# Kernel optimization log

Measured on AMD Instinct MI355X. Metric: run time of the kernel, lower is better.

The kernel has to match this reference:

```python
import jax, jax.numpy as jnp
import numpy as np

# Fixed-step Dormand-Prince RK45 (dopri5) over t in [0, 1].
# torchdiffeq's dopri5 is adaptive; an adaptive while-loop is not
# reverse-differentiable in JAX, so we use the same dopri5 tableau with a
# fixed step count, which reproduces the per-step math exactly.
N_STEPS = 64

# dopri5 Butcher tableau (a-matrix rows; b = 5th-order weights = row a7)
A21 = 1/5
A31, A32 = 3/40, 9/40
A41, A42, A43 = 44/45, -56/15, 32/9
A51, A52, A53, A54 = 19372/6561, -25360/2187, 64448/6561, -212/729
A61, A62, A63, A64, A65 = 9017/3168, -355/33, 46732/5247, 49/176, -5103/18656
B1, B3, B4, B5, B6 = 35/384, 500/1113, 125/192, -2187/6784, 11/84


def setup_inputs() -> dict:
    key = jax.random.key(0)
    ks = jax.random.split(key, 7)
    data_dim, hidden_dim, batch = 512, 1024, 4096
    s1 = 1.0 / np.sqrt(data_dim)
    s2 = 1.0 / np.sqrt(hidden_dim)
    return {
        "x":  jax.random.normal(ks[0], (batch, data_dim), jnp.float32),
        "W1": jax.random.normal(ks[1], (hidden_dim, data_dim), jnp.float32) * s1,
        "b1": jax.random.normal(ks[2], (hidden_dim,), jnp.float32) * s1,
        "W2": jax.random.normal(ks[3], (hidden_dim, hidden_dim), jnp.float32) * s2,
        "b2": jax.random.normal(ks[4], (hidden_dim,), jnp.float32) * s2,
        "W3": jax.random.normal(ks[5], (data_dim, hidden_dim), jnp.float32) * s2,
        "b3": jax.random.normal(ks[6], (data_dim,), jnp.float32) * s2,
    }


def reference(x, W1, b1, W2, b2, W3, b3):
    def f(y):  # ODEFunc MLP: fc1 -> relu -> fc2 -> relu -> fc3 (autonomous)
        h = jax.nn.relu(y @ W1.T + b1)
        h = jax.nn.relu(h @ W2.T + b2)
        return h @ W3.T + b3

    h = jnp.float32(1.0 / N_STEPS)

    def step(y, _):
        k1 = f(y)
        k2 = f(y + h * (A21 * k1))
        k3 = f(y + h * (A31 * k1 + A32 * k2))
        k4 = f(y + h * (A41 * k1 + A42 * k2 + A43 * k3))
        k5 = f(y + h * (A51 * k1 + A52 * k2 + A53 * k3 + A54 * k4))
        k6 = f(y + h * (A61 * k1 + A62 * k2 + A63 * k3 + A64 * k4 + A65 * k5))
        y_next = y + h * (B1 * k1 + B3 * k3 + B4 * k4 + B5 * k5 + B6 * k6)
        return y_next, None

    y_final, _ = jax.lax.scan(step, x, None, length=N_STEPS)
    return y_final
```

## Files before the change

### kernel.cpp

```cpp
#include <hip/hip_runtime.h>
#include <hip/hip_bf16.h>
#include <stdint.h>
#include <stddef.h>

using bf16_t = __hip_bfloat16;
typedef __attribute__((ext_vector_type(8))) short short8;
typedef __attribute__((ext_vector_type(4))) float f32x4;

__device__ __forceinline__ void gload_lds16(void* lds, const void* g) {
  __builtin_amdgcn_global_load_lds(
      (const __attribute__((address_space(1))) unsigned int*)g,
      (__attribute__((address_space(3))) unsigned int*)lds,
      16, 0, 0);
}

template<int MFRAG, bool RELU, bool COMBINE, bool STORE_K, bool STORE_YF>
__global__ __launch_bounds__(256, 2)
void gemm_bt(const bf16_t* __restrict__ A, const bf16_t* __restrict__ B,
             const float* __restrict__ bias,
             bf16_t* __restrict__ obf,
             float* __restrict__ kout,
             float* __restrict__ yf_out,
             const float* __restrict__ y_in,
             const float* __restrict__ kp0, const float* __restrict__ kp1,
             const float* __restrict__ kp2, const float* __restrict__ kp3,
             float c0, float c1, float c2, float c3, float ccur,
             int M, int N, int K, int lgx)
{
  constexpr int BM = 32 * MFRAG;
  constexpr int BN = 64;
  constexpr int NFRAG = 2;
  constexpr int AR = BM / 32;
  constexpr int BR = 2;
  constexpr int LPT = AR + BR;

  __shared__ __align__(16) bf16_t As[3][BM * 64];
  __shared__ __align__(16) bf16_t Bs[3][BN * 64];

  const int t    = threadIdx.x;
  const int lane = t & 63;
  const int wid  = t >> 6;
  const int wm   = wid >> 1;
  const int wn   = wid & 1;

  const int nwg = gridDim.x;
  const int bid = blockIdx.x;
  const int swz = (bid & 7) * (nwg >> 3) + (bid >> 3);
  const int gxm = (1 << lgx) - 1;
  const int bx  = swz & gxm;
  const int by  = swz >> lgx;

  const int bn0 = bx * BN;
  const int bm0 = by * BM;

  const bf16_t* Ag = A + (size_t)bm0 * K;
  const bf16_t* Bg = B + (size_t)bn0 * K;

  f32x4 acc[MFRAG][NFRAG] = {};

  auto stage = [&](int b, int kt) {
    const int k0 = kt * 64;
#pragma unroll
    for (int r = 0; r < AR; ++r) {
      int ch  = t + r * 256;
      int row = ch >> 3, s = ch & 7;
      int sl  = s ^ (row & 7);
      gload_lds16(&As[b][ch * 8], Ag + (size_t)row * K + k0 + sl * 8);
    }
#pragma unroll
    for (int r = 0; r < BR; ++r) {
      int ch  = t + r * 256;
      int row = ch >> 3, s = ch & 7;
      int sl  = s ^ (row & 7);
      gload_lds16(&Bs[b][ch * 8], Bg + (size_t)row * K + k0 + sl * 8);
    }
  };

  const int nt = K >> 6;
  stage(0, 0);
  stage(1, 1);

  const int ro = lane & 15;
  const int ks = lane >> 4;

  int c = 0;
  for (int tt = 0; tt < nt; ++tt) {
    if (tt == nt - 1) {
      asm volatile("s_waitcnt vmcnt(0)" ::: "memory");
    } else if constexpr (LPT == 6) {
      asm volatile("s_waitcnt vmcnt(6)" ::: "memory");
    } else {
      asm volatile("s_waitcnt vmcnt(4)" ::: "memory");
    }
    __builtin_amdgcn_s_barrier();
    asm volatile("" ::: "memory");

#pragma unroll
    for (int kk = 0; kk < 2; ++kk) {
      short8 af[MFRAG], bfr[NFRAG];
      const int slot = kk * 4 + ks;
#pragma unroll
      for (int mi = 0; mi < MFRAG; ++mi) {
        int row = wm * (MFRAG * 16) + mi * 16 + ro;
        int ch  = row * 8 + (slot ^ (row & 7));
        af[mi]  = *(const short8*)&As[c][ch * 8];
      }
#pragma unroll
      for (int ni = 0; ni < NFRAG; ++ni) {
        int row = wn * 32 + ni * 16 + ro;
        int ch  = row * 8 + (slot ^ (row & 7));
        bfr[ni] = *(const short8*)&Bs[c][ch * 8];
      }
#pragma unroll
      for (int mi = 0; mi < MFRAG; ++mi)
#pragma unroll
        for (int ni = 0; ni < NFRAG; ++ni)
          acc[mi][ni] = __builtin_amdgcn_mfma_f32_16x16x32_bf16(
              af[mi], bfr[ni], acc[mi][ni], 0, 0, 0);
    }

    asm volatile("" ::: "memory");
    __builtin_amdgcn_s_barrier();
    asm volatile("" ::: "memory");

    if (tt + 2 < nt) {
      int nb = c + 2; if (nb >= 3) nb -= 3;
      stage(nb, tt + 2);
    }
    if (++c == 3) c = 0;
  }

  const int rb = bm0 + wm * (MFRAG * 16);
  const int cb = bn0 + wn * 32;
#pragma unroll
  for (int mi = 0; mi < MFRAG; ++mi) {
#pragma unroll
    for (int ni = 0; ni < NFRAG; ++ni) {
      const int col = cb + ni * 16 + (lane & 15);
      const float bv = bias[col];
#pragma unroll
      for (int r = 0; r < 4; ++r) {
        const int row = rb + mi * 16 + (lane >> 4) * 4 + r;
        const size_t idx = (size_t)row * N + col;
        float v = acc[mi][ni][r] + bv;
        if (RELU) v = fmaxf(v, 0.f);
        if (COMBINE) {
          if (STORE_K) kout[idx] = v;
          float z = y_in[idx] + ccur * v;
          if (kp0) z += c0 * kp0[idx];
          if (kp1) z += c1 * kp1[idx];
          if (kp2) z += c2 * kp2[idx];
          if (kp3) z += c3 * kp3[idx];
          if (STORE_YF) yf_out[idx] = z;
          obf[idx] = __float2bfloat16(z);
        } else {
          obf[idx] = __float2bfloat16(v);
        }
      }
    }
  }
}

__global__ void init_y_kernel(const float* __restrict__ x, float* __restrict__ y,
                              bf16_t* __restrict__ yb, int n) {
  int i = blockIdx.x * blockDim.x + threadIdx.x;
  if (i < n) {
    float v = x[i];
    y[i]  = v;
    yb[i] = __float2bfloat16(v);
  }
}

__global__ void f2b_kernel(const float* __restrict__ in, bf16_t* __restrict__ out, int n) {
  int i = blockIdx.x * blockDim.x + threadIdx.x;
  if (i < n) out[i] = __float2bfloat16(in[i]);
}

extern "C" void kernel_launch(void* const* d_in, const int* in_sizes, int n_in,
                              void* d_out, int out_size, void* d_ws, size_t ws_size,
                              hipStream_t stream)
{
  const float* x  = (const float*)d_in[0];
  const float* W1 = (const float*)d_in[1];
  const float* b1 = (const float*)d_in[2];
  const float* W2 = (const float*)d_in[3];
  const float* b2 = (const float*)d_in[4];
  const float* W3 = (const float*)d_in[5];
  const float* b3 = (const float*)d_in[6];

  const int data   = in_sizes[6];
  const int hidden = in_sizes[2];
  const int batch  = in_sizes[0] / data;

  char* ws = (char*)d_ws;
  size_t off = 0;
  auto alloc = [&](size_t bytes) -> void* {
    off = (off + 255) & ~(size_t)255;
    void* p = ws + off;
    off += bytes;
    return p;
  };
  const size_t nyd = (size_t)batch * data;
  const size_t nh  = (size_t)batch * hidden;

  float*  y   = (float*)alloc(nyd * 4);
  bf16_t* yb  = (bf16_t*)alloc(nyd * 2);
  bf16_t* zb  = (bf16_t*)alloc(nyd * 2);
  bf16_t* h1  = (bf16_t*)alloc(nh * 2);
  bf16_t* h2  = (bf16_t*)alloc(nh * 2);
  float*  k1  = (float*)alloc(nyd * 4);
  float*  k2  = (float*)alloc(nyd * 4);
  float*  k3  = (float*)alloc(nyd * 4);
  float*  k4  = (float*)alloc(nyd * 4);
  float*  k5  = (float*)alloc(nyd * 4);
  bf16_t* W1b = (bf16_t*)alloc((size_t)hidden * data * 2);
  bf16_t* W2b = (bf16_t*)alloc((size_t)hidden * hidden * 2);
  bf16_t* W3b = (bf16_t*)alloc((size_t)data * hidden * 2);

  {
    int n = (int)nyd;
    init_y_kernel<<<(n + 255) / 256, 256, 0, stream>>>(x, y, yb, n);
    n = hidden * data;
    f2b_kernel<<<(n + 255) / 256, 256, 0, stream>>>(W1, W1b, n);
    n = hidden * hidden;
    f2b_kernel<<<(n + 255) / 256, 256, 0, stream>>>(W2, W2b, n);
    n = data * hidden;
    f2b_kernel<<<(n + 255) / 256, 256, 0, stream>>>(W3, W3b, n);
  }

  const double hh = 1.0 / 64.0;
  const float hA21 = (float)(hh * (1.0/5.0));
  const float hA31 = (float)(hh * (3.0/40.0)),    hA32 = (float)(hh * (9.0/40.0));
  const float hA41 = (float)(hh * (44.0/45.0)),   hA42 = (float)(hh * (-56.0/15.0)),
              hA43 = (float)(hh * (32.0/9.0));
  const float hA51 = (float)(hh * (19372.0/6561.0)),  hA52 = (float)(hh * (-25360.0/2187.0)),
              hA53 = (float)(hh * (64448.0/6561.0)),  hA54 = (float)(hh * (-212.0/729.0));
  const float hA61 = (float)(hh * (9017.0/3168.0)),   hA62 = (float)(hh * (-355.0/33.0)),
              hA63 = (float)(hh * (46732.0/5247.0)),  hA64 = (float)(hh * (49.0/176.0)),
              hA65 = (float)(hh * (-5103.0/18656.0));
  const float hB1 = (float)(hh * (35.0/384.0)),   hB3 = (float)(hh * (500.0/1113.0)),
              hB4 = (float)(hh * (125.0/192.0)),  hB5 = (float)(hh * (-2187.0/6784.0)),
              hB6 = (float)(hh * (11.0/84.0));

  const dim3 blk(256);
  const int gridH = (hidden / 64) * (batch / 128);
  const int grid3 = (data / 64) * (batch / 64);
  const int lgxH = 4, lgx3 = 3;

  auto mlp_front = [&](const bf16_t* zin) {
    gemm_bt<4, true, false, false, false><<<gridH, blk, 0, stream>>>(
        zin, W1b, b1, h1, nullptr, nullptr, nullptr,
        nullptr, nullptr, nullptr, nullptr, 0.f, 0.f, 0.f, 0.f, 0.f,
        batch, hidden, data, lgxH);
    gemm_bt<4, true, false, false, false><<<gridH, blk, 0, stream>>>(
        h1, W2b, b2, h2, nullptr, nullptr, nullptr,
        nullptr, nullptr, nullptr, nullptr, 0.f, 0.f, 0.f, 0.f, 0.f,
        batch, hidden, hidden, lgxH);
  };

  auto stage_k = [&](float* kout, const float* p0, float cc0, const float* p1, float cc1,
                     const float* p2, float cc2, const float* p3, float cc3, float ccur) {
    gemm_bt<2, false, true, true, false><<<grid3, blk, 0, stream>>>(
        h2, W3b, b3, zb, kout, nullptr, y,
        p0, p1, p2, p3, cc0, cc1, cc2, cc3, ccur,
        batch, data, hidden, lgx3);
  };

  for (int step = 0; step < 64; ++step) {
    mlp_front(yb);
    stage_k(k1, nullptr, 0.f, nullptr, 0.f, nullptr, 0.f, nullptr, 0.f, hA21);
    mlp_front(zb);
    stage_k(k2, k1, hA31, nullptr, 0.f, nullptr, 0.f, nullptr, 0.f, hA32);
    mlp_front(zb);
    stage_k(k3, k1, hA41, k2, hA42, nullptr, 0.f, nullptr, 0.f, hA43);
    mlp_front(zb);
    stage_k(k4, k1, hA51, k2, hA52, k3, hA53, nullptr, 0.f, hA54);
    mlp_front(zb);
    stage_k(k5, k1, hA61, k2, hA62, k3, hA63, k4, hA64, hA65);
    mlp_front(zb);
    float* yf = (step == 63) ? (float*)d_out : y;
    gemm_bt<2, false, true, false, true><<<grid3, blk, 0, stream>>>(
        h2, W3b, b3, yb, nullptr, yf, y,
        k1, k3, k4, k5, hB1, hB3, hB4, hB5, hB6,
        batch, data, hidden, lgx3);
  }
}
```

Measured before the change: 18.49 ms.

## Drop second barrier, prefetch earlier, raise MFMA priority, store RK stages in bf16

```diff
diff --git a/kernel.cpp b/kernel.cpp
--- a/kernel.cpp
+++ b/kernel.cpp
@@ -19,11 +19,11 @@
 void gemm_bt(const bf16_t* __restrict__ A, const bf16_t* __restrict__ B,
              const float* __restrict__ bias,
              bf16_t* __restrict__ obf,
-             float* __restrict__ kout,
+             bf16_t* __restrict__ kout,
              float* __restrict__ yf_out,
              const float* __restrict__ y_in,
-             const float* __restrict__ kp0, const float* __restrict__ kp1,
-             const float* __restrict__ kp2, const float* __restrict__ kp3,
+             const bf16_t* __restrict__ kp0, const bf16_t* __restrict__ kp1,
+             const bf16_t* __restrict__ kp2, const bf16_t* __restrict__ kp3,
              float c0, float c1, float c2, float c3, float ccur,
              int M, int N, int K, int lgx)
 {
@@ -43,15 +43,12 @@
   const int wm   = wid >> 1;
   const int wn   = wid & 1;
 
-  const int nwg = gridDim.x;
-  const int bid = blockIdx.x;
+  const int nwg = gridDim.x, bid = blockIdx.x;
   const int swz = (bid & 7) * (nwg >> 3) + (bid >> 3);
   const int gxm = (1 << lgx) - 1;
   const int bx  = swz & gxm;
   const int by  = swz >> lgx;
-
-  const int bn0 = bx * BN;
-  const int bm0 = by * BM;
+  const int bn0 = bx * BN, bm0 = by * BM;
 
   const bf16_t* Ag = A + (size_t)bm0 * K;
   const bf16_t* Bg = B + (size_t)bn0 * K;
@@ -95,6 +92,11 @@
     __builtin_amdgcn_s_barrier();
     asm volatile("" ::: "memory");
 
+    if (tt + 2 < nt) {
+      int nb = c + 2; if (nb >= 3) nb -= 3;
+      stage(nb, tt + 2);
+    }
+
 #pragma unroll
     for (int kk = 0; kk < 2; ++kk) {
       short8 af[MFRAG], bfr[NFRAG];
@@ -111,22 +113,16 @@
         int ch  = row * 8 + (slot ^ (row & 7));
         bfr[ni] = *(const short8*)&Bs[c][ch * 8];
       }
+      __builtin_amdgcn_s_setprio(1);
 #pragma unroll
       for (int mi = 0; mi < MFRAG; ++mi)
 #pragma unroll
         for (int ni = 0; ni < NFRAG; ++ni)
           acc[mi][ni] = __builtin_amdgcn_mfma_f32_16x16x32_bf16(
               af[mi], bfr[ni], acc[mi][ni], 0, 0, 0);
-    }
-
-    asm volatile("" ::: "memory");
-    __builtin_amdgcn_s_barrier();
-    asm volatile("" ::: "memory");
-
-    if (tt + 2 < nt) {
-      int nb = c + 2; if (nb >= 3) nb -= 3;
-      stage(nb, tt + 2);
-    }
+      __builtin_amdgcn_s_setprio(0);
+    }
+
     if (++c == 3) c = 0;
   }
 
@@ -136,7 +132,7 @@
   for (int mi = 0; mi < MFRAG; ++mi) {
 #pragma unroll
     for (int ni = 0; ni < NFRAG; ++ni) {
-      const int col = cb + ni * 16 + (lane & 15);
+      const int col = cb + ni * 16 + ro;
       const float bv = bias[col];
 #pragma unroll
       for (int r = 0; r < 4; ++r) {
@@ -145,12 +141,12 @@
         float v = acc[mi][ni][r] + bv;
         if (RELU) v = fmaxf(v, 0.f);
         if (COMBINE) {
-          if (STORE_K) kout[idx] = v;
+          if (STORE_K) kout[idx] = __float2bfloat16(v);
           float z = y_in[idx] + ccur * v;
-          if (kp0) z += c0 * kp0[idx];
-          if (kp1) z += c1 * kp1[idx];
-          if (kp2) z += c2 * kp2[idx];
-          if (kp3) z += c3 * kp3[idx];
+          if (kp0) z += c0 * __bfloat162float(kp0[idx]);
+          if (kp1) z += c1 * __bfloat162float(kp1[idx]);
+          if (kp2) z += c2 * __bfloat162float(kp2[idx]);
+          if (kp3) z += c3 * __bfloat162float(kp3[idx]);
           if (STORE_YF) yf_out[idx] = z;
           obf[idx] = __float2bfloat16(z);
         } else {
@@ -208,11 +204,11 @@
   bf16_t* zb  = (bf16_t*)alloc(nyd * 2);
   bf16_t* h1  = (bf16_t*)alloc(nh * 2);
   bf16_t* h2  = (bf16_t*)alloc(nh * 2);
-  float*  k1  = (float*)alloc(nyd * 4);
-  float*  k2  = (float*)alloc(nyd * 4);
-  float*  k3  = (float*)alloc(nyd * 4);
-  float*  k4  = (float*)alloc(nyd * 4);
-  float*  k5  = (float*)alloc(nyd * 4);
+  bf16_t* k1  = (bf16_t*)alloc(nyd * 2);
+  bf16_t* k2  = (bf16_t*)alloc(nyd * 2);
+  bf16_t* k3  = (bf16_t*)alloc(nyd * 2);
+  bf16_t* k4  = (bf16_t*)alloc(nyd * 2);
+  bf16_t* k5  = (bf16_t*)alloc(nyd * 2);
   bf16_t* W1b = (bf16_t*)alloc((size_t)hidden * data * 2);
   bf16_t* W2b = (bf16_t*)alloc((size_t)hidden * hidden * 2);
   bf16_t* W3b = (bf16_t*)alloc((size_t)data * hidden * 2);
@@ -258,8 +254,8 @@
         batch, hidden, hidden, lgxH);
   };
 
-  auto stage_k = [&](float* kout, const float* p0, float cc0, const float* p1, float cc1,
-                     const float* p2, float cc2, const float* p3, float cc3, float ccur) {
+  auto stage_k = [&](bf16_t* kout, const bf16_t* p0, float cc0, const bf16_t* p1, float cc1,
+                     const bf16_t* p2, float cc2, const bf16_t* p3, float cc3, float ccur) {
     gemm_bt<2, false, true, true, false><<<grid3, blk, 0, stream>>>(
         h2, W3b, b3, zb, kout, nullptr, y,
         p0, p1, p2, p3, cc0, cc1, cc2, cc3, ccur,
```

Result: no change. 18.72 ms (+1.2%).
